# Kernel tuning notes

Measured on AMD Instinct MI355X. Metric: run time of the kernel, lower is better.

Reference implementation:

```python
import jax, jax.numpy as jnp
import numpy as np

B, L, H, W, C = 2, 5, 48, 176, 256
HEADS, DIM_HEAD = 8, 32
INNER = HEADS * DIM_HEAD  # 256
SCALE = DIM_HEAD ** -0.5


def setup_inputs() -> dict:
    key = jax.random.key(0)
    k1, k2, k3, k4, k5 = jax.random.split(key, 5)
    x = jax.random.normal(k1, (B, L, H, W, C), dtype=jnp.float32)
    # mask of shape (B, H, W, 1, L); slot 0 always valid so no softmax row is fully masked
    mask = jax.random.randint(k2, (B, H, W, 1, L), 0, 2, dtype=jnp.int32)
    mask = mask.at[..., 0].set(1)
    w_qkv = jax.random.normal(k3, (C, 3 * INNER), dtype=jnp.float32) / np.sqrt(C)
    w_out = jax.random.normal(k4, (INNER, C), dtype=jnp.float32) / np.sqrt(INNER)
    b_out = jax.random.normal(k5, (C,), dtype=jnp.float32) * 0.01
    return {"x": x, "mask": mask, "w_qkv": w_qkv, "w_out": w_out, "b_out": b_out}


def reference(x, mask, w_qkv, w_out, b_out):
    # x: (B, L, H, W, C) -> (B, H, W, L, C)
    xp = jnp.transpose(x, (0, 2, 3, 1, 4))
    qkv = xp @ w_qkv  # (B, H, W, L, 3*INNER)
    q, k, v = jnp.split(qkv, 3, axis=-1)
    # split heads: (B, H, W, L, M, D)
    shp = (B, H, W, L, HEADS, DIM_HEAD)
    q = q.reshape(shp)
    k = k.reshape(shp)
    v = v.reshape(shp)
    # attention over the small CAV axis L
    att = jnp.einsum('bhwimd,bhwjmd->bmhwij', q, k) * SCALE  # (B,M,H,W,L,L)
    m = mask[:, None]  # (B,1,H,W,1,L) broadcasts over (B,M,H,W,i,j)
    att = jnp.where(m == 0, -jnp.inf, att)
    att = jax.nn.softmax(att, axis=-1)
    out = jnp.einsum('bmhwij,bhwjmd->bhwimd', att, v)  # (B,H,W,L,M,D)
    out = out.reshape(B, H, W, L, INNER)
    out = out @ w_out + b_out  # dropout is identity in eval
    return jnp.transpose(out, (0, 3, 1, 2, 4))  # (B, L, H, W, C)
```

## Files before the change

### kernel.cpp

```cpp
#include <hip/hip_runtime.h>


typedef __attribute__((ext_vector_type(8))) short short8;
typedef __attribute__((ext_vector_type(4))) float f32x4;

#define SCALE_F 0.17677669529663687f

static __device__ __forceinline__ float b2f(unsigned short u) {
    union { unsigned u; float f; } x; x.u = ((unsigned)u) << 16; return x.f;
}
static __device__ __forceinline__ unsigned short f2b(float f) {
    union { float f; unsigned u; } x; x.f = f;
    unsigned u = x.u;
    return (unsigned short)((u + 0x7FFFu + ((u >> 16) & 1u)) >> 16);
}
static __device__ __forceinline__ unsigned pk_bf16(float lo, float hi) {
    unsigned u;
    asm("v_cvt_pk_bf16_f32 %0, %1, %2" : "=v"(u) : "v"(lo), "v"(hi));
    return u;
}

static __device__ __forceinline__ size_t row_to_xoff(int r) {
    int l = r % 5; int t = r / 5;
    int w = t % 176; t /= 176;
    int h = t % 48; int b = t / 48;
    return (size_t)(((b * 5 + l) * 48 + h) * 176 + w) * 256;
}

static __device__ __forceinline__ int lidx(int r, int c) {
    return r * 256 + ((((c >> 3) ^ (r & 7)) << 3) | (c & 7));
}

static __device__ __forceinline__ void async_cp16(const unsigned short* g, unsigned short* l) {
    __builtin_amdgcn_global_load_lds(
        (__attribute__((address_space(1))) void*)(void*)g,
        (__attribute__((address_space(3))) void*)(void*)l, 16, 0, 0);
}

static __device__ __forceinline__ void wait_lgkm() {
    __builtin_amdgcn_s_waitcnt(0xC07F);
}

static __device__ __forceinline__ void barrier_lgkm() {
    __builtin_amdgcn_s_waitcnt(0xC07F);
    __builtin_amdgcn_s_barrier();
}

__global__ __launch_bounds__(256) void k_prep(const float* __restrict__ wq,
                                              const float* __restrict__ wo,
                                              unsigned short* __restrict__ wqt,
                                              unsigned short* __restrict__ wot) {
    __shared__ unsigned short tile[64 * 65];
    const int bb = blockIdx.x;
    const float* src; unsigned short* dst; int kt, nt, ncols;
    if (bb < 48) { kt = bb / 12; nt = bb % 12; src = wq; dst = wqt; ncols = 768; }
    else { int b2 = bb - 48; kt = b2 >> 2; nt = b2 & 3; src = wo; dst = wot; ncols = 256; }
    const int t = threadIdx.x;
#pragma unroll
    for (int p = 0; p < 4; ++p) {
        int u = p * 256 + t; int r = u >> 4, c4 = u & 15;
        float4 v = *(const float4*)&src[(size_t)(kt * 64 + r) * ncols + nt * 64 + c4 * 4];
        tile[r * 65 + c4 * 4 + 0] = f2b(v.x);
        tile[r * 65 + c4 * 4 + 1] = f2b(v.y);
        tile[r * 65 + c4 * 4 + 2] = f2b(v.z);
        tile[r * 65 + c4 * 4 + 3] = f2b(v.w);
    }
    __syncthreads();
#pragma unroll
    for (int p = 0; p < 2; ++p) {
        int u = p * 256 + t; int n = u >> 3, c8 = u & 7;
        short8 o;
#pragma unroll
        for (int j = 0; j < 8; ++j) o[j] = (short)tile[(c8 * 8 + j) * 65 + n];
        *(short8*)&dst[(nt * 64 + n) * 256 + kt * 64 + c8 * 8] = o;
    }
}

template<int C>
static __device__ __forceinline__ void issue_chunk(const unsigned short* __restrict__ wqt,
                                                   const unsigned short* __restrict__ wot,
                                                   unsigned short* __restrict__ Bw,
                                                   int n0w, int lane) {
    constexpr int sel = (C < 24) ? (C % 3) : 3;
    constexpr int kk  = (C < 24) ? (C / 3) : (C - 24);
    constexpr int slot = C & 1;
    const unsigned short* wbase = (sel < 3) ? (wqt + sel * 65536) : wot;
#pragma unroll
    for (int t = 0; t < 2; ++t) {
        int cidx = t * 64 + lane;
        int nl = cidx >> 2;
        int kq = (cidx & 3) ^ ((nl >> 1) & 3);
        const unsigned short* g = wbase + (n0w + nl) * 256 + kk * 32 + kq * 8;
        async_cp16(g, Bw + slot * 1024 + t * 512);
    }
}

#define MFMA_ALL(ACC)                                                               \
    _Pragma("unroll")                                                               \
    for (int m = 0; m < 5; ++m)                                                     \
        _Pragma("unroll")                                                           \
        for (int n = 0; n < 2; ++n)                                                 \
            ACC[m][n] = __builtin_amdgcn_mfma_f32_16x16x32_bf16(a[m], b[n], ACC[m][n], 0, 0, 0);

template<int C>
static __device__ __forceinline__ void qkv_step(f32x4 (&aq)[5][2], f32x4 (&ak)[5][2],
        f32x4 (&av)[5][2], short8 (&a)[5],
        const unsigned short* __restrict__ As, unsigned short* __restrict__ Bw,
        const unsigned short* __restrict__ wqt, const unsigned short* __restrict__ wot,
        int n0w, int lane) {
    constexpr int sel = C % 3;
    constexpr int kk = C / 3;
    constexpr int slot = C & 1;
    const int ln = lane & 15, quad = lane >> 4;
    __builtin_amdgcn_s_waitcnt(0xF72);
    short8 b[2];
#pragma unroll
    for (int n = 0; n < 2; ++n)
        b[n] = *(const short8*)&Bw[slot * 1024 + (n * 16 + ln) * 32
                                   + ((quad ^ ((ln >> 1) & 3)) * 8)];
    __builtin_amdgcn_s_waitcnt(0xC07F);
    if constexpr (C + 2 < 32) issue_chunk<C + 2>(wqt, wot, Bw, n0w, lane);
    if constexpr (sel == 0) {
#pragma unroll
        for (int m = 0; m < 5; ++m)
            a[m] = *(const short8*)&As[lidx(m * 16 + ln, kk * 32 + quad * 8)];
    }
    if constexpr (sel == 0) { MFMA_ALL(aq) } else if constexpr (sel == 1) { MFMA_ALL(ak) }
    else { MFMA_ALL(av) }
}

template<int C>
static __device__ __forceinline__ void out_step(f32x4 (&ao)[5][2],
        const unsigned short* __restrict__ As, unsigned short* __restrict__ Bw,
        const unsigned short* __restrict__ wqt, const unsigned short* __restrict__ wot,
        int n0w, int lane) {
    constexpr int kk = C - 24;
    constexpr int slot = C & 1;
    constexpr int imm = (C == 31) ? 0xF70 : 0xF72;
    const int ln = lane & 15, quad = lane >> 4;
    __builtin_amdgcn_s_waitcnt(imm);
    short8 b[2];
#pragma unroll
    for (int n = 0; n < 2; ++n)
        b[n] = *(const short8*)&Bw[slot * 1024 + (n * 16 + ln) * 32
                                   + ((quad ^ ((ln >> 1) & 3)) * 8)];
    __builtin_amdgcn_s_waitcnt(0xC07F);
    if constexpr (C + 2 < 32) issue_chunk<C + 2>(wqt, wot, Bw, n0w, lane);
    short8 a[5];
#pragma unroll
    for (int m = 0; m < 5; ++m)
        a[m] = *(const short8*)&As[lidx(m * 16 + ln, kk * 32 + quad * 8)];
    MFMA_ALL(ao)
}

static __device__ __forceinline__ void cstore(const f32x4 (&acc)[5][2],
        unsigned short* __restrict__ Ds, int n0w, int lane) {
    const int ln = lane & 15, quad = lane >> 4;
#pragma unroll
    for (int m = 0; m < 5; ++m)
#pragma unroll
        for (int n = 0; n < 2; ++n) {
            const int col = n0w + n * 16 + ln, r0 = m * 16 + quad * 4;
            unsigned p01 = pk_bf16(acc[m][n][0], acc[m][n][1]);
            unsigned p23 = pk_bf16(acc[m][n][2], acc[m][n][3]);
            Ds[lidx(r0 + 0, col)] = (unsigned short)p01;
            Ds[lidx(r0 + 1, col)] = (unsigned short)(p01 >> 16);
            Ds[lidx(r0 + 2, col)] = (unsigned short)p23;
            Ds[lidx(r0 + 3, col)] = (unsigned short)(p23 >> 16);
        }
}

__global__ __launch_bounds__(512, 2) void k_fused(const float* __restrict__ x,
                                                  const int* __restrict__ mask,
                                                  const unsigned short* __restrict__ wqt,
                                                  const unsigned short* __restrict__ wot,
                                                  const float* __restrict__ bo,
                                                  float* __restrict__ out) {
    __shared__ __align__(16) unsigned short xs[80 * 256];
    __shared__ __align__(16) unsigned short qs[80 * 256];
    __shared__ __align__(16) unsigned short kvs[80 * 256];
    __shared__ __align__(16) unsigned short Bb[8 * 2048];

    const int tid = threadIdx.x;
    const int blk = blockIdx.x;
    const int rbase = blk * 80;
    const int lane = tid & 63, wv = tid >> 6;
    const int n0w = wv * 32;
    const int ln = lane & 15, quad = lane >> 4;
    unsigned short* Bw = Bb + wv * 2048;

#pragma unroll
    for (int i = 0; i < 5; ++i) {
        int u = i * 512 + tid;
        int r = u >> 5, cb = u & 31;
        size_t xo = row_to_xoff(rbase + r) + cb * 8;
        float4 v0 = *(const float4*)(x + xo);
        float4 v1 = *(const float4*)(x + xo + 4);
        int4 o;
        o.x = (int)pk_bf16(v0.x, v0.y);
        o.y = (int)pk_bf16(v0.z, v0.w);
        o.z = (int)pk_bf16(v1.x, v1.y);
        o.w = (int)pk_bf16(v1.z, v1.w);
        *(int4*)&xs[lidx(r, cb * 8)] = o;
    }

    const int part = lane & 3, g = lane >> 2;
    const int c0 = n0w + part * 8;
    int mk[5];
#pragma unroll
    for (int j = 0; j < 5; ++j) mk[j] = mask[(blk * 16 + g) * 5 + j];

    issue_chunk<0>(wqt, wot, Bw, n0w, lane);
    issue_chunk<1>(wqt, wot, Bw, n0w, lane);

    barrier_lgkm();

    f32x4 aq[5][2], ak[5][2], av[5][2];
#pragma unroll
    for (int m = 0; m < 5; ++m)
#pragma unroll
        for (int n = 0; n < 2; ++n) {
            aq[m][n] = (f32x4){0.f, 0.f, 0.f, 0.f};
            ak[m][n] = (f32x4){0.f, 0.f, 0.f, 0.f};
            av[m][n] = (f32x4){0.f, 0.f, 0.f, 0.f};
        }
    {
        short8 a[5];
        qkv_step<0>(aq, ak, av, a, xs, Bw, wqt, wot, n0w, lane);
        qkv_step<1>(aq, ak, av, a, xs, Bw, wqt, wot, n0w, lane);
        qkv_step<2>(aq, ak, av, a, xs, Bw, wqt, wot, n0w, lane);
        qkv_step<3>(aq, ak, av, a, xs, Bw, wqt, wot, n0w, lane);
        qkv_step<4>(aq, ak, av, a, xs, Bw, wqt, wot, n0w, lane);
        qkv_step<5>(aq, ak, av, a, xs, Bw, wqt, wot, n0w, lane);
        qkv_step<6>(aq, ak, av, a, xs, Bw, wqt, wot, n0w, lane);
        qkv_step<7>(aq, ak, av, a, xs, Bw, wqt, wot, n0w, lane);
        qkv_step<8>(aq, ak, av, a, xs, Bw, wqt, wot, n0w, lane);
        qkv_step<9>(aq, ak, av, a, xs, Bw, wqt, wot, n0w, lane);
        qkv_step<10>(aq, ak, av, a, xs, Bw, wqt, wot, n0w, lane);
        qkv_step<11>(aq, ak, av, a, xs, Bw, wqt, wot, n0w, lane);
        qkv_step<12>(aq, ak, av, a, xs, Bw, wqt, wot, n0w, lane);
        qkv_step<13>(aq, ak, av, a, xs, Bw, wqt, wot, n0w, lane);
        qkv_step<14>(aq, ak, av, a, xs, Bw, wqt, wot, n0w, lane);
        qkv_step<15>(aq, ak, av, a, xs, Bw, wqt, wot, n0w, lane);
        qkv_step<16>(aq, ak, av, a, xs, Bw, wqt, wot, n0w, lane);
        qkv_step<17>(aq, ak, av, a, xs, Bw, wqt, wot, n0w, lane);
        qkv_step<18>(aq, ak, av, a, xs, Bw, wqt, wot, n0w, lane);
        qkv_step<19>(aq, ak, av, a, xs, Bw, wqt, wot, n0w, lane);
        qkv_step<20>(aq, ak, av, a, xs, Bw, wqt, wot, n0w, lane);
        qkv_step<21>(aq, ak, av, a, xs, Bw, wqt, wot, n0w, lane);
        qkv_step<22>(aq, ak, av, a, xs, Bw, wqt, wot, n0w, lane);
        qkv_step<23>(aq, ak, av, a, xs, Bw, wqt, wot, n0w, lane);
    }
    cstore(aq, qs, n0w, lane);
    cstore(ak, kvs, n0w, lane);
    wait_lgkm();

    float pr[5][5];
    {
        float qf[5][8];
#pragma unroll
        for (int i = 0; i < 5; ++i) {
            short8 qv = *(const short8*)&qs[lidx(g * 5 + i, c0)];
#pragma unroll
            for (int d = 0; d < 8; ++d) qf[i][d] = b2f((unsigned short)qv[d]);
        }
        float s[5][5];
#pragma unroll
        for (int j = 0; j < 5; ++j) {
            short8 kv = *(const short8*)&kvs[lidx(g * 5 + j, c0)];
            float kf[8];
#pragma unroll
            for (int d = 0; d < 8; ++d) kf[d] = b2f((unsigned short)kv[d]);
#pragma unroll
            for (int i = 0; i < 5; ++i) {
                float acc = 0.f;
#pragma unroll
                for (int d = 0; d < 8; ++d) acc += qf[i][d] * kf[d];
                s[i][j] = acc;
            }
        }
#pragma unroll
        for (int i = 0; i < 5; ++i)
#pragma unroll
            for (int j = 0; j < 5; ++j) {
                s[i][j] += __shfl_xor(s[i][j], 1, 64);
                s[i][j] += __shfl_xor(s[i][j], 2, 64);
            }
#pragma unroll
        for (int i = 0; i < 5; ++i) {
            float mx = -1e30f;
#pragma unroll
            for (int j = 0; j < 5; ++j) {
                s[i][j] = mk[j] ? s[i][j] * SCALE_F : -1e30f;
                mx = fmaxf(mx, s[i][j]);
            }
            float sum = 0.f;
#pragma unroll
            for (int j = 0; j < 5; ++j) { pr[i][j] = __expf(s[i][j] - mx); sum += pr[i][j]; }
            float inv = 1.f / sum;
#pragma unroll
            for (int j = 0; j < 5; ++j) pr[i][j] *= inv;
        }
    }
    wait_lgkm();

    cstore(av, kvs, n0w, lane);
    wait_lgkm();

    {
        float o[5][8];
#pragma unroll
        for (int i = 0; i < 5; ++i)
#pragma unroll
            for (int d = 0; d < 8; ++d) o[i][d] = 0.f;
#pragma unroll
        for (int j = 0; j < 5; ++j) {
            short8 vv = *(const short8*)&kvs[lidx(g * 5 + j, c0)];
            float vf[8];
#pragma unroll
            for (int d = 0; d < 8; ++d) vf[d] = b2f((unsigned short)vv[d]);
#pragma unroll
            for (int i = 0; i < 5; ++i)
#pragma unroll
                for (int d = 0; d < 8; ++d) o[i][d] += pr[i][j] * vf[d];
        }
#pragma unroll
        for (int i = 0; i < 5; ++i) {
            int4 ov;
            ov.x = (int)pk_bf16(o[i][0], o[i][1]);
            ov.y = (int)pk_bf16(o[i][2], o[i][3]);
            ov.z = (int)pk_bf16(o[i][4], o[i][5]);
            ov.w = (int)pk_bf16(o[i][6], o[i][7]);
            *(int4*)&kvs[lidx(g * 5 + i, c0)] = ov;
        }
    }
    barrier_lgkm();

    {
        f32x4 ao[5][2];
#pragma unroll
        for (int m = 0; m < 5; ++m)
#pragma unroll
            for (int n = 0; n < 2; ++n) ao[m][n] = (f32x4){0.f, 0.f, 0.f, 0.f};
        out_step<24>(ao, kvs, Bw, wqt, wot, n0w, lane);
        out_step<25>(ao, kvs, Bw, wqt, wot, n0w, lane);
        out_step<26>(ao, kvs, Bw, wqt, wot, n0w, lane);
        out_step<27>(ao, kvs, Bw, wqt, wot, n0w, lane);
        out_step<28>(ao, kvs, Bw, wqt, wot, n0w, lane);
        out_step<29>(ao, kvs, Bw, wqt, wot, n0w, lane);
        out_step<30>(ao, kvs, Bw, wqt, wot, n0w, lane);
        out_step<31>(ao, kvs, Bw, wqt, wot, n0w, lane);
        float bv2[2];
#pragma unroll
        for (int n = 0; n < 2; ++n) bv2[n] = bo[n0w + n * 16 + ln];
#pragma unroll
        for (int m = 0; m < 5; ++m)
#pragma unroll
            for (int rg = 0; rg < 4; ++rg) {
                int row = m * 16 + quad * 4 + rg;
                size_t off = row_to_xoff(rbase + row);
#pragma unroll
                for (int n = 0; n < 2; ++n)
                    out[off + n0w + n * 16 + ln] = ao[m][n][rg] + bv2[n];
            }
    }
}

extern "C" void kernel_launch(void* const* d_in, const int* in_sizes, int n_in,
                              void* d_out, int out_size, void* d_ws, size_t ws_size,
                              hipStream_t stream) {
    const float* x   = (const float*)d_in[0];
    const int* mask  = (const int*)d_in[1];
    const float* wq  = (const float*)d_in[2];
    const float* wo  = (const float*)d_in[3];
    const float* bo  = (const float*)d_in[4];
    float* out = (float*)d_out;

    char* ws = (char*)d_ws;
    unsigned short* wqt = (unsigned short*)(ws);
    unsigned short* wot = (unsigned short*)(ws + 393216);

    hipLaunchKernelGGL(k_prep, dim3(64), dim3(256), 0, stream, wq, wo, wqt, wot);
    hipLaunchKernelGGL(k_fused, dim3(1056), dim3(512), 0, stream, x, mask, wqt, wot, bo, out);
}
```

Before: 239.5 us.

## Load weight fragments directly into registers via 3-deep ring instead of LDS staging

```diff
diff --git a/kernel.cpp b/kernel.cpp
--- a/kernel.cpp
+++ b/kernel.cpp
@@ -29,12 +29,6 @@
 
 static __device__ __forceinline__ int lidx(int r, int c) {
     return r * 256 + ((((c >> 3) ^ (r & 7)) << 3) | (c & 7));
-}
-
-static __device__ __forceinline__ void async_cp16(const unsigned short* g, unsigned short* l) {
-    __builtin_amdgcn_global_load_lds(
-        (__attribute__((address_space(1))) void*)(void*)g,
-        (__attribute__((address_space(3))) void*)(void*)l, 16, 0, 0);
 }
 
 static __device__ __forceinline__ void wait_lgkm() {
@@ -77,22 +71,15 @@
 }
 
 template<int C>
-static __device__ __forceinline__ void issue_chunk(const unsigned short* __restrict__ wqt,
-                                                   const unsigned short* __restrict__ wot,
-                                                   unsigned short* __restrict__ Bw,
-                                                   int n0w, int lane) {
-    constexpr int sel = (C < 24) ? (C % 3) : 3;
-    constexpr int kk  = (C < 24) ? (C / 3) : (C - 24);
-    constexpr int slot = C & 1;
-    const unsigned short* wbase = (sel < 3) ? (wqt + sel * 65536) : wot;
-#pragma unroll
-    for (int t = 0; t < 2; ++t) {
-        int cidx = t * 64 + lane;
-        int nl = cidx >> 2;
-        int kq = (cidx & 3) ^ ((nl >> 1) & 3);
-        const unsigned short* g = wbase + (n0w + nl) * 256 + kk * 32 + kq * 8;
-        async_cp16(g, Bw + slot * 1024 + t * 512);
-    }
+static __device__ __forceinline__ void load_chunk(short8 (&ring)[3][2],
+        const unsigned short* __restrict__ wq_l,
+        const unsigned short* __restrict__ wo_l) {
+    constexpr int sel  = (C < 24) ? (C % 3) : 3;
+    constexpr int kk   = (C < 24) ? (C / 3) : (C - 24);
+    constexpr int slot = C % 3;
+    const unsigned short* base = (sel < 3) ? (wq_l + sel * 65536) : wo_l;
+    ring[slot][0] = *(const short8*)&base[kk * 32];
+    ring[slot][1] = *(const short8*)&base[4096 + kk * 32];
 }
 
 #define MFMA_ALL(ACC)                                                               \
@@ -104,53 +91,48 @@
 
 template<int C>
 static __device__ __forceinline__ void qkv_step(f32x4 (&aq)[5][2], f32x4 (&ak)[5][2],
-        f32x4 (&av)[5][2], short8 (&a)[5],
-        const unsigned short* __restrict__ As, unsigned short* __restrict__ Bw,
-        const unsigned short* __restrict__ wqt, const unsigned short* __restrict__ wot,
-        int n0w, int lane) {
+        f32x4 (&av)[5][2], short8 (&a)[5], short8 (&ring)[3][2],
+        const unsigned short* __restrict__ As,
+        const unsigned short* __restrict__ wq_l, const unsigned short* __restrict__ wo_l,
+        int lane) {
     constexpr int sel = C % 3;
     constexpr int kk = C / 3;
-    constexpr int slot = C & 1;
+    constexpr int slot = C % 3;
     const int ln = lane & 15, quad = lane >> 4;
-    __builtin_amdgcn_s_waitcnt(0xF72);
     short8 b[2];
-#pragma unroll
-    for (int n = 0; n < 2; ++n)
-        b[n] = *(const short8*)&Bw[slot * 1024 + (n * 16 + ln) * 32
-                                   + ((quad ^ ((ln >> 1) & 3)) * 8)];
-    __builtin_amdgcn_s_waitcnt(0xC07F);
-    if constexpr (C + 2 < 32) issue_chunk<C + 2>(wqt, wot, Bw, n0w, lane);
+    b[0] = ring[slot][0];
+    b[1] = ring[slot][1];
+    if constexpr (C + 3 < 32) load_chunk<C + 3>(ring, wq_l, wo_l);
     if constexpr (sel == 0) {
 #pragma unroll
         for (int m = 0; m < 5; ++m)
             a[m] = *(const short8*)&As[lidx(m * 16 + ln, kk * 32 + quad * 8)];
     }
+    __builtin_amdgcn_s_setprio(1);
     if constexpr (sel == 0) { MFMA_ALL(aq) } else if constexpr (sel == 1) { MFMA_ALL(ak) }
     else { MFMA_ALL(av) }
+    __builtin_amdgcn_s_setprio(0);
 }
 
 template<int C>
-static __device__ __forceinline__ void out_step(f32x4 (&ao)[5][2],
-        const unsigned short* __restrict__ As, unsigned short* __restrict__ Bw,
-        const unsigned short* __restrict__ wqt, const unsigned short* __restrict__ wot,
-        int n0w, int lane) {
+static __device__ __forceinline__ void out_step(f32x4 (&ao)[5][2], short8 (&ring)[3][2],
+        const unsigned short* __restrict__ As,
+        const unsigned short* __restrict__ wq_l, const unsigned short* __restrict__ wo_l,
+        int lane) {
     constexpr int kk = C - 24;
-    constexpr int slot = C & 1;
-    constexpr int imm = (C == 31) ? 0xF70 : 0xF72;
+    constexpr int slot = C % 3;
     const int ln = lane & 15, quad = lane >> 4;
-    __builtin_amdgcn_s_waitcnt(imm);
     short8 b[2];
-#pragma unroll
-    for (int n = 0; n < 2; ++n)
-        b[n] = *(const short8*)&Bw[slot * 1024 + (n * 16 + ln) * 32
-                                   + ((quad ^ ((ln >> 1) & 3)) * 8)];
-    __builtin_amdgcn_s_waitcnt(0xC07F);
-    if constexpr (C + 2 < 32) issue_chunk<C + 2>(wqt, wot, Bw, n0w, lane);
+    b[0] = ring[slot][0];
+    b[1] = ring[slot][1];
+    if constexpr (C + 3 < 32) load_chunk<C + 3>(ring, wq_l, wo_l);
     short8 a[5];
 #pragma unroll
     for (int m = 0; m < 5; ++m)
         a[m] = *(const short8*)&As[lidx(m * 16 + ln, kk * 32 + quad * 8)];
+    __builtin_amdgcn_s_setprio(1);
     MFMA_ALL(ao)
+    __builtin_amdgcn_s_setprio(0);
 }
 
 static __device__ __forceinline__ void cstore(const f32x4 (&acc)[5][2],
@@ -179,7 +161,6 @@
     __shared__ __align__(16) unsigned short xs[80 * 256];
     __shared__ __align__(16) unsigned short qs[80 * 256];
     __shared__ __align__(16) unsigned short kvs[80 * 256];
-    __shared__ __align__(16) unsigned short Bb[8 * 2048];
 
     const int tid = threadIdx.x;
     const int blk = blockIdx.x;
@@ -187,7 +168,14 @@
     const int lane = tid & 63, wv = tid >> 6;
     const int n0w = wv * 32;
     const int ln = lane & 15, quad = lane >> 4;
-    unsigned short* Bw = Bb + wv * 2048;
+
+    const unsigned short* wq_l = wqt + (n0w + ln) * 256 + quad * 8;
+    const unsigned short* wo_l = wot + (n0w + ln) * 256 + quad * 8;
+
+    short8 ring[3][2];
+    load_chunk<0>(ring, wq_l, wo_l);
+    load_chunk<1>(ring, wq_l, wo_l);
+    load_chunk<2>(ring, wq_l, wo_l);
 
 #pragma unroll
     for (int i = 0; i < 5; ++i) {
@@ -210,9 +198,6 @@
 #pragma unroll
     for (int j = 0; j < 5; ++j) mk[j] = mask[(blk * 16 + g) * 5 + j];
 
-    issue_chunk<0>(wqt, wot, Bw, n0w, lane);
-    issue_chunk<1>(wqt, wot, Bw, n0w, lane);
-
     barrier_lgkm();
 
     f32x4 aq[5][2], ak[5][2], av[5][2];
@@ -226,30 +211,30 @@
         }
     {
         short8 a[5];
-        qkv_step<0>(aq, ak, av, a, xs, Bw, wqt, wot, n0w, lane);
-        qkv_step<1>(aq, ak, av, a, xs, Bw, wqt, wot, n0w, lane);
-        qkv_step<2>(aq, ak, av, a, xs, Bw, wqt, wot, n0w, lane);
-        qkv_step<3>(aq, ak, av, a, xs, Bw, wqt, wot, n0w, lane);
-        qkv_step<4>(aq, ak, av, a, xs, Bw, wqt, wot, n0w, lane);
-        qkv_step<5>(aq, ak, av, a, xs, Bw, wqt, wot, n0w, lane);
-        qkv_step<6>(aq, ak, av, a, xs, Bw, wqt, wot, n0w, lane);
-        qkv_step<7>(aq, ak, av, a, xs, Bw, wqt, wot, n0w, lane);
-        qkv_step<8>(aq, ak, av, a, xs, Bw, wqt, wot, n0w, lane);
-        qkv_step<9>(aq, ak, av, a, xs, Bw, wqt, wot, n0w, lane);
-        qkv_step<10>(aq, ak, av, a, xs, Bw, wqt, wot, n0w, lane);
-        qkv_step<11>(aq, ak, av, a, xs, Bw, wqt, wot, n0w, lane);
-        qkv_step<12>(aq, ak, av, a, xs, Bw, wqt, wot, n0w, lane);
-        qkv_step<13>(aq, ak, av, a, xs, Bw, wqt, wot, n0w, lane);
-        qkv_step<14>(aq, ak, av, a, xs, Bw, wqt, wot, n0w, lane);
-        qkv_step<15>(aq, ak, av, a, xs, Bw, wqt, wot, n0w, lane);
-        qkv_step<16>(aq, ak, av, a, xs, Bw, wqt, wot, n0w, lane);
-        qkv_step<17>(aq, ak, av, a, xs, Bw, wqt, wot, n0w, lane);
-        qkv_step<18>(aq, ak, av, a, xs, Bw, wqt, wot, n0w, lane);
-        qkv_step<19>(aq, ak, av, a, xs, Bw, wqt, wot, n0w, lane);
-        qkv_step<20>(aq, ak, av, a, xs, Bw, wqt, wot, n0w, lane);
-        qkv_step<21>(aq, ak, av, a, xs, Bw, wqt, wot, n0w, lane);
-        qkv_step<22>(aq, ak, av, a, xs, Bw, wqt, wot, n0w, lane);
-        qkv_step<23>(aq, ak, av, a, xs, Bw, wqt, wot, n0w, lane);
+        qkv_step<0>(aq, ak, av, a, ring, xs, wq_l, wo_l, lane);
+        qkv_step<1>(aq, ak, av, a, ring, xs, wq_l, wo_l, lane);
+        qkv_step<2>(aq, ak, av, a, ring, xs, wq_l, wo_l, lane);
+        qkv_step<3>(aq, ak, av, a, ring, xs, wq_l, wo_l, lane);
+        qkv_step<4>(aq, ak, av, a, ring, xs, wq_l, wo_l, lane);
+        qkv_step<5>(aq, ak, av, a, ring, xs, wq_l, wo_l, lane);
+        qkv_step<6>(aq, ak, av, a, ring, xs, wq_l, wo_l, lane);
+        qkv_step<7>(aq, ak, av, a, ring, xs, wq_l, wo_l, lane);
+        qkv_step<8>(aq, ak, av, a, ring, xs, wq_l, wo_l, lane);
+        qkv_step<9>(aq, ak, av, a, ring, xs, wq_l, wo_l, lane);
+        qkv_step<10>(aq, ak, av, a, ring, xs, wq_l, wo_l, lane);
+        qkv_step<11>(aq, ak, av, a, ring, xs, wq_l, wo_l, lane);
+        qkv_step<12>(aq, ak, av, a, ring, xs, wq_l, wo_l, lane);
+        qkv_step<13>(aq, ak, av, a, ring, xs, wq_l, wo_l, lane);
+        qkv_step<14>(aq, ak, av, a, ring, xs, wq_l, wo_l, lane);
+        qkv_step<15>(aq, ak, av, a, ring, xs, wq_l, wo_l, lane);
+        qkv_step<16>(aq, ak, av, a, ring, xs, wq_l, wo_l, lane);
+        qkv_step<17>(aq, ak, av, a, ring, xs, wq_l, wo_l, lane);
+        qkv_step<18>(aq, ak, av, a, ring, xs, wq_l, wo_l, lane);
+        qkv_step<19>(aq, ak, av, a, ring, xs, wq_l, wo_l, lane);
+        qkv_step<20>(aq, ak, av, a, ring, xs, wq_l, wo_l, lane);
+        qkv_step<21>(aq, ak, av, a, ring, xs, wq_l, wo_l, lane);
+        qkv_step<22>(aq, ak, av, a, ring, xs, wq_l, wo_l, lane);
+        qkv_step<23>(aq, ak, av, a, ring, xs, wq_l, wo_l, lane);
     }
     cstore(aq, qs, n0w, lane);
     cstore(ak, kvs, n0w, lane);
@@ -342,14 +327,14 @@
         for (int m = 0; m < 5; ++m)
 #pragma unroll
             for (int n = 0; n < 2; ++n) ao[m][n] = (f32x4){0.f, 0.f, 0.f, 0.f};
-        out_step<24>(ao, kvs, Bw, wqt, wot, n0w, lane);
-        out_step<25>(ao, kvs, Bw, wqt, wot, n0w, lane);
-        out_step<26>(ao, kvs, Bw, wqt, wot, n0w, lane);
-        out_step<27>(ao, kvs, Bw, wqt, wot, n0w, lane);
-        out_step<28>(ao, kvs, Bw, wqt, wot, n0w, lane);
-        out_step<29>(ao, kvs, Bw, wqt, wot, n0w, lane);
-        out_step<30>(ao, kvs, Bw, wqt, wot, n0w, lane);
-        out_step<31>(ao, kvs, Bw, wqt, wot, n0w, lane);
+        out_step<24>(ao, ring, kvs, wq_l, wo_l, lane);
+        out_step<25>(ao, ring, kvs, wq_l, wo_l, lane);
+        out_step<26>(ao, ring, kvs, wq_l, wo_l, lane);
+        out_step<27>(ao, ring, kvs, wq_l, wo_l, lane);
+        out_step<28>(ao, ring, kvs, wq_l, wo_l, lane);
+        out_step<29>(ao, ring, kvs, wq_l, wo_l, lane);
+        out_step<30>(ao, ring, kvs, wq_l, wo_l, lane);
+        out_step<31>(ao, ring, kvs, wq_l, wo_l, lane);
         float bv2[2];
 #pragma unroll
         for (int n = 0; n < 2; ++n) bv2[n] = bo[n0w + n * 16 + ln];
```

New measurement: 255.1 us. 1.07x slower.
